# Kernel optimization log

Measured on AMD Instinct MI355X. Metric: run time of the kernel, lower is better.

Reference implementation:

```python
import jax, jax.numpy as jnp
import numpy as np

B, T, J, C = 32, 256, 21, 3
BT = B * T
N = BT * J

_TPL_SRC = np.array([0, 1, 2, 3, 4, 0, 5, 6, 7, 8, 0, 9, 10, 11, 12, 0, 13, 14, 15, 16, 0, 17, 18, 19, 20], np.int32)
_TPL_DST = np.array([1, 2, 3, 4, 0, 5, 6, 7, 8, 0, 9, 10, 11, 12, 0, 13, 14, 15, 16, 0, 17, 18, 19, 20, 0], np.int32)


def _build_edges():
    off = (np.arange(BT, dtype=np.int32) * J)[:, None]
    src = (_TPL_SRC[None, :] + off).ravel()
    dst = (_TPL_DST[None, :] + off).ravel()
    # PyG GATConv default add_self_loops=True (both layers see the same augmented set)
    loops = np.arange(N, dtype=np.int32)
    return np.concatenate([src, loops]), np.concatenate([dst, loops])


def setup_inputs() -> dict:
    key = jax.random.key(0)
    ks = jax.random.split(key, 8)
    src, dst = _build_edges()
    return {
        "keypoints": jax.random.normal(ks[0], (B, T, J, C), jnp.float32),
        "W1": jax.random.normal(ks[1], (3, 256), jnp.float32) * 0.3,
        "att1_src": jax.random.normal(ks[2], (4, 64), jnp.float32) * 0.1,
        "att1_dst": jax.random.normal(ks[3], (4, 64), jnp.float32) * 0.1,
        "b1": jnp.zeros((256,), jnp.float32),
        "W2": jax.random.normal(ks[4], (256, 128), jnp.float32) * 0.06,
        "att2_src": jax.random.normal(ks[5], (1, 128), jnp.float32) * 0.1,
        "att2_dst": jax.random.normal(ks[6], (1, 128), jnp.float32) * 0.1,
        "b2": jnp.zeros((128,), jnp.float32),
        "src": jnp.asarray(src),
        "dst": jnp.asarray(dst),
    }


def _gat_conv(x, src, dst, W, a_src, a_dst, b, heads, d_head):
    n = x.shape[0]
    h = (x @ W).reshape(n, heads, d_head)            # [N,H,D]
    e_s = jnp.einsum('nhd,hd->nh', h, a_src)          # [N,H]
    e_d = jnp.einsum('nhd,hd->nh', h, a_dst)
    e = jax.nn.leaky_relu(e_s[src] + e_d[dst], 0.2)   # [E,H]
    m = jax.ops.segment_max(e, dst, num_segments=n)
    ex = jnp.exp(e - m[dst])
    z = jax.ops.segment_sum(ex, dst, num_segments=n)
    alpha = ex / z[dst]                               # scatter-softmax over dst
    out = jax.ops.segment_sum(h[src] * alpha[:, :, None], dst, num_segments=n)
    return out.reshape(n, heads * d_head) + b


def reference(keypoints, W1, att1_src, att1_dst, b1, W2, att2_src, att2_dst, b2, src, dst):
    x = keypoints.reshape(N, C)
    x = jax.nn.relu(_gat_conv(x, src, dst, W1, att1_src, att1_dst, b1, 4, 64))
    x = jax.nn.relu(_gat_conv(x, src, dst, W2, att2_src, att2_dst, b2, 1, 128))
    x = x.reshape(BT, J, 128).mean(axis=1)            # pool joints
    return x.reshape(B, T, 128).mean(axis=1)          # pool time -> [B,128]
```

## Files before the change

kernel.cpp:

```cpp
#include <hip/hip_runtime.h>

#define NJ  21
#define X1S 264
#define H2S 132
#define XAS 40

typedef __attribute__((ext_vector_type(8))) short  bf16x8;
typedef __attribute__((ext_vector_type(4))) float  floatx4;

__device__ __forceinline__ float lrelu(float v){ return v > 0.f ? v : 0.2f*v; }
__device__ __forceinline__ unsigned short f2bf(float x){
  unsigned int u = __float_as_uint(x);
  return (unsigned short)((u + 0x7FFFu + ((u >> 16) & 1u)) >> 16);
}
__device__ __forceinline__ unsigned short f2bf_u(float x){
  return (unsigned short)((__float_as_uint(x) + 0x8000u) >> 16);
}

__global__ void prep(const float* __restrict__ W1, const float* __restrict__ a1s,
                     const float* __restrict__ a1d, const float* __restrict__ W2,
                     unsigned short* __restrict__ w2f, unsigned short* __restrict__ w1b,
                     float* __restrict__ ws1o, float* __restrict__ out){
  const int t = threadIdx.x, b = blockIdx.x;
  if (b < 32){
    int base = b*1024 + t*4;
    #pragma unroll
    for (int i = 0; i < 4; ++i){
      int idx = base + i;
      int j = idx & 7, lane = (idx >> 3) & 63, nt = (idx >> 9) & 7, kt = idx >> 12;
      int k = kt*32 + (lane >> 4)*8 + j;
      int n = nt*16 + (lane & 15);
      w2f[idx] = f2bf(W2[k*128 + n]);
    }
  } else if (b < 40){
    int base = (b - 32)*1024 + t*4;
    #pragma unroll
    for (int i = 0; i < 4; ++i){
      int idx = base + i;
      int j = idx & 7, lane = (idx >> 3) & 63, nt = idx >> 9;
      int k = (lane >> 4)*8 + j;
      int n = nt*16 + (lane & 15);
      float v = 0.f;
      if (k < 16){
        int h = k >> 2, c = k & 3;
        if (c < 3 && h == (n >> 6)) v = W1[c*256 + n];
      }
      w1b[idx] = f2bf(v);
    }
  } else {
    if (t < 24){
      int c = t % 3, h = (t/3) & 3, sd = t/12;
      const float* av = sd ? a1d : a1s;
      float s = 0.f;
      #pragma unroll
      for (int d = 0; d < 64; ++d) s += W1[c*256 + h*64 + d]*av[h*64 + d];
      ws1o[sd*12 + c*4 + h] = s;
    }
    for (int i = t; i < 4096; i += 256) out[i] = 0.f;
  }
}

__global__ __launch_bounds__(256, 5)
void gat_fused(const float* __restrict__ kp,  const float* __restrict__ b1v,
               const float* __restrict__ a2s, const float* __restrict__ a2d,
               const float* __restrict__ b2v, const unsigned short* __restrict__ w2f,
               const unsigned short* __restrict__ w1b, const float* __restrict__ ws1g,
               float* __restrict__ out)
{
  __shared__ float xsL[2][NJ][4];
  __shared__ unsigned short xagb[48*XAS] __attribute__((aligned(16)));
  __shared__ float a2sL[128], a2dL[128];
  __shared__ unsigned short x1bf[48*X1S] __attribute__((aligned(16)));
  float* h2f = (float*)x1bf;
  float* esL = (float*)xagb;
  float* edL = (float*)((char*)xagb + 176);
  float (*al2F)[NJ][8] = (float(*)[NJ][8])((char*)xagb + 352);

  const int t = threadIdx.x, blk = blockIdx.x;
  const int w = t >> 6, lane = t & 63, quad = lane >> 4, ln15 = lane & 15;
  const int h = t & 3;

  if (t < 126){ int fl = t >= 63; int r = t - 63*fl; xsL[fl][r/3][r%3] = kp[blk*126 + t]; }
  if (t < 128) a2sL[t] = a2s[t]; else a2dL[t-128] = a2d[t-128];
  __syncthreads();

  if (t < 168){
    int fn = t >> 2, fl = fn >= NJ, n = fn - fl*NJ;
    float wsr[3], wdr[3];
    #pragma unroll
    for (int c = 0; c < 3; ++c){ wsr[c] = ws1g[c*4 + h]; wdr[c] = ws1g[12 + c*4 + h]; }
    int p[6], np;
    if (n == 0){ p[0]=4;p[1]=8;p[2]=12;p[3]=16;p[4]=20;p[5]=0; np=6; }
    else       { p[0]=(n%4==1)?0:(n-1); p[1]=n; np=2; }
    float4 xself = *(const float4*)&xsL[fl][n][0];
    float ed = xself.x*wdr[0] + xself.y*wdr[1] + xself.z*wdr[2];
    float4 xp[6]; float e[6]; float m = -1e30f;
    for (int i = 0; i < np; ++i){
      xp[i] = *(const float4*)&xsL[fl][p[i]][0];
      float es = xp[i].x*wsr[0] + xp[i].y*wsr[1] + xp[i].z*wsr[2];
      e[i] = lrelu(es + ed); m = fmaxf(m, e[i]);
    }
    float z = 0.f;
    for (int i = 0; i < np; ++i){ e[i] = __expf(e[i]-m); z += e[i]; }
    float inv = 1.f/z;
    float a0 = 0.f, a1 = 0.f, a2v = 0.f;
    for (int i = 0; i < np; ++i){
      float al = e[i]*inv;
      a0 += al*xp[i].x; a1 += al*xp[i].y; a2v += al*xp[i].z;
    }
    uint2 pk;
    pk.x = (unsigned)f2bf(a0) | ((unsigned)f2bf(a1) << 16);
    pk.y = (unsigned)f2bf(a2v);
    *(uint2*)&xagb[fn*XAS + h*4] = pk;
    uint2 z2; z2.x = 0u; z2.y = 0u;
    *(uint2*)&xagb[fn*XAS + 16 + h*4] = z2;
  }
  __syncthreads();

  {
    bf16x8 A0 = *(bf16x8*)&xagb[(     ln15)*XAS + quad*8];
    bf16x8 A1 = *(bf16x8*)&xagb[(16 + ln15)*XAS + quad*8];
    bf16x8 A2 = *(bf16x8*)&xagb[(32 + ln15)*XAS + quad*8];
    bf16x8 Bv[4]; float bb[4];
    #pragma unroll
    for (int i = 0; i < 4; ++i){
      Bv[i] = *(const bf16x8*)(w1b + (unsigned)((w*4 + i)*64 + lane)*8);
      bb[i] = b1v[w*64 + i*16 + ln15];
    }
    #pragma unroll
    for (int i = 0; i < 4; ++i){
      const int cb = w*64 + i*16 + ln15;
      floatx4 c0 = {0.f,0.f,0.f,0.f}, c1 = c0, c2 = c0;
      c0 = __builtin_amdgcn_mfma_f32_16x16x32_bf16(A0, Bv[i], c0, 0,0,0);
      c1 = __builtin_amdgcn_mfma_f32_16x16x32_bf16(A1, Bv[i], c1, 0,0,0);
      c2 = __builtin_amdgcn_mfma_f32_16x16x32_bf16(A2, Bv[i], c2, 0,0,0);
      #pragma unroll
      for (int r = 0; r < 4; ++r){
        x1bf[(     quad*4 + r)*X1S + cb] = f2bf_u(fmaxf(c0[r] + bb[i], 0.f));
        x1bf[(16 + quad*4 + r)*X1S + cb] = f2bf_u(fmaxf(c1[r] + bb[i], 0.f));
        x1bf[(32 + quad*4 + r)*X1S + cb] = f2bf_u(fmaxf(c2[r] + bb[i], 0.f));
      }
    }
  }
  __syncthreads();

  floatx4 acc[3][2];
  #pragma unroll
  for (int mt = 0; mt < 3; ++mt){ acc[mt][0] = (floatx4){0.f,0.f,0.f,0.f}; acc[mt][1] = acc[mt][0]; }
  {
    #define LDA(row0, kt) (*(bf16x8*)&x1bf[((row0) + ln15)*X1S + (kt)*32 + quad*8])
    #define LDB(kt, half) (*(const bf16x8*)(w2f + (unsigned)(((kt)*8 + 2*w + (half))*64 + lane)*8))
    bf16x8 A0c = LDA(0,0), A1c = LDA(16,0), A2c = LDA(32,0);
    bf16x8 B0s[3], B1s[3];
    #pragma unroll
    for (int i = 0; i < 3; ++i){ B0s[i] = LDB(i,0); B1s[i] = LDB(i,1); }
    #pragma unroll
    for (int kt = 0; kt < 8; ++kt){
      bf16x8 b0c = B0s[kt%3], b1c = B1s[kt%3];
      bf16x8 A0n, A1n, A2n;
      if (kt < 7){ A0n = LDA(0,kt+1); A1n = LDA(16,kt+1); A2n = LDA(32,kt+1); }
      if (kt < 5){ B0s[kt%3] = LDB(kt+3,0); B1s[kt%3] = LDB(kt+3,1); }
      acc[0][0] = __builtin_amdgcn_mfma_f32_16x16x32_bf16(A0c, b0c, acc[0][0], 0,0,0);
      acc[0][1] = __builtin_amdgcn_mfma_f32_16x16x32_bf16(A0c, b1c, acc[0][1], 0,0,0);
      acc[1][0] = __builtin_amdgcn_mfma_f32_16x16x32_bf16(A1c, b0c, acc[1][0], 0,0,0);
      acc[1][1] = __builtin_amdgcn_mfma_f32_16x16x32_bf16(A1c, b1c, acc[1][1], 0,0,0);
      acc[2][0] = __builtin_amdgcn_mfma_f32_16x16x32_bf16(A2c, b0c, acc[2][0], 0,0,0);
      acc[2][1] = __builtin_amdgcn_mfma_f32_16x16x32_bf16(A2c, b1c, acc[2][1], 0,0,0);
      if (kt < 7){ A0c = A0n; A1c = A1n; A2c = A2n; }
    }
    #undef LDA
    #undef LDB
  }
  __syncthreads();
  {
    const int c0 = 32*w + ln15, c1 = c0 + 16;
    #pragma unroll
    for (int mt = 0; mt < 3; ++mt){
      #pragma unroll
      for (int r = 0; r < 4; ++r){
        int row = mt*16 + quad*4 + r;
        if (row < 42){
          h2f[row*H2S + c0] = acc[mt][0][r];
          h2f[row*H2S + c1] = acc[mt][1][r];
        }
      }
    }
  }
  __syncthreads();

  if (w < 2){
    const int fl = w;
    float s = 0.f, d = 0.f;
    if (lane < 42){
      int n = lane >> 1, cb2 = (lane & 1)*64;
      const float* hp  = h2f + (fl*NJ + n)*H2S + cb2;
      const float* asp = a2sL + cb2;
      const float* adp = a2dL + cb2;
      #pragma unroll
      for (int c = 0; c < 64; c += 4){
        float4 hv = *(const float4*)(hp + c);
        float4 av = *(const float4*)(asp + c);
        float4 dv = *(const float4*)(adp + c);
        s += hv.x*av.x + hv.y*av.y + hv.z*av.z + hv.w*av.w;
        d += hv.x*dv.x + hv.y*dv.y + hv.z*dv.z + hv.w*dv.w;
      }
    }
    s += __shfl_xor(s, 1); d += __shfl_xor(d, 1);
    if (lane < 42 && (lane & 1) == 0){ esL[fl*NJ + (lane>>1)] = s; edL[fl*NJ + (lane>>1)] = d; }
    __threadfence_block();
    if (lane < NJ){
      int n = lane;
      int p[6], np;
      if (n == 0){ p[0]=4;p[1]=8;p[2]=12;p[3]=16;p[4]=20;p[5]=0; np=6; }
      else       { p[0]=(n%4==1)?0:(n-1); p[1]=n; np=2; }
      float ed = edL[fl*NJ + n];
      float e[6], m = -1e30f;
      for (int i = 0; i < np; ++i){ e[i] = lrelu(esL[fl*NJ + p[i]] + ed); m = fmaxf(m, e[i]); }
      float z = 0.f;
      for (int i = 0; i < np; ++i){ e[i] = __expf(e[i]-m); z += e[i]; }
      float inv = 1.f/z;
      for (int i = 0; i < np; ++i) al2F[fl][n][i] = e[i]*inv;
    }
    __threadfence_block();
    #pragma unroll
    for (int jj = 0; jj < 2; ++jj){
      int j = lane + jj*64;
      float bj = b2v[j];
      float h0 = h2f[(fl*NJ)*H2S + j];
      float v0 = al2F[fl][0][5]*h0;
      float sum = 0.f, hprev = h0;
      #pragma unroll
      for (int n = 1; n < NJ; ++n){
        float hn = h2f[(fl*NJ + n)*H2S + j];
        float pv = ((n & 3) == 1) ? h0 : hprev;
        float2 al = *(const float2*)&al2F[fl][n][0];
        sum += fmaxf(bj + al.x*pv + al.y*hn, 0.f);
        if ((n & 3) == 0) v0 += al2F[fl][0][(n >> 2) - 1]*hn;
        hprev = hn;
      }
      sum += fmaxf(bj + v0, 0.f);
      atomicAdd(&out[(blk >> 7)*128 + j], sum*(1.f/5376.f));
    }
  }
}

extern "C" void kernel_launch(void* const* d_in, const int* in_sizes, int n_in,
                              void* d_out, int out_size, void* d_ws, size_t ws_size,
                              hipStream_t stream){
  const float* kp  = (const float*)d_in[0];
  const float* W1  = (const float*)d_in[1];
  const float* a1s = (const float*)d_in[2];
  const float* a1d = (const float*)d_in[3];
  const float* b1  = (const float*)d_in[4];
  const float* W2  = (const float*)d_in[5];
  const float* a2s = (const float*)d_in[6];
  const float* a2d = (const float*)d_in[7];
  const float* b2  = (const float*)d_in[8];
  float* out = (float*)d_out;

  unsigned short* w2f = (unsigned short*)d_ws;
  unsigned short* w1b = (unsigned short*)((char*)d_ws + 65536);
  float* ws1 = (float*)((char*)d_ws + 65536 + 16384);

  prep<<<41, 256, 0, stream>>>(W1, a1s, a1d, W2, w2f, w1b, ws1, out);
  gat_fused<<<4096, 256, 0, stream>>>(kp, b1, a2s, a2d, b2, w2f, w1b, ws1, out);
}
```

Baseline: 139.9 us.

## Restructure GAT kernel to one wave per frame with barrier-free execution

Each block is now a single 64-thread wave that processes one frame of 21 joints, where before it was four waves handling two frames. All __syncthreads become __threadfence_block, and the wave computes the full 256-wide layer-1 output and all 128 layer-2 columns with 16 accumulators. The aim is to remove block-level barriers and pad waste (48 rows down to 32), and to raise the number of independent blocks. In exchange, each wave reloads all of W2 from global or L2 with no split across waves, and register pressure rises. Atomic contention on the output also doubles.

New measurement: 185.6 us. 32.7% more time.

```diff
diff --git a/kernel.cpp b/kernel.cpp
--- a/kernel.cpp
+++ b/kernel.cpp
@@ -60,142 +60,117 @@
   }
 }
 
-__global__ __launch_bounds__(256, 5)
+__global__ __launch_bounds__(64, 3)
 void gat_fused(const float* __restrict__ kp,  const float* __restrict__ b1v,
                const float* __restrict__ a2s, const float* __restrict__ a2d,
                const float* __restrict__ b2v, const unsigned short* __restrict__ w2f,
                const unsigned short* __restrict__ w1b, const float* __restrict__ ws1g,
                float* __restrict__ out)
 {
-  __shared__ float xsL[2][NJ][4];
-  __shared__ unsigned short xagb[48*XAS] __attribute__((aligned(16)));
-  __shared__ float a2sL[128], a2dL[128];
-  __shared__ unsigned short x1bf[48*X1S] __attribute__((aligned(16)));
+  __shared__ unsigned short x1bf[NJ*X1S] __attribute__((aligned(16)));
+  __shared__ float xs[NJ][4];
+  __shared__ unsigned short xagb[32*XAS] __attribute__((aligned(16)));
+  __shared__ float esL[NJ], edL[NJ];
+  __shared__ float al2[NJ][6];
   float* h2f = (float*)x1bf;
-  float* esL = (float*)xagb;
-  float* edL = (float*)((char*)xagb + 176);
-  float (*al2F)[NJ][8] = (float(*)[NJ][8])((char*)xagb + 352);
-
-  const int t = threadIdx.x, blk = blockIdx.x;
-  const int w = t >> 6, lane = t & 63, quad = lane >> 4, ln15 = lane & 15;
-  const int h = t & 3;
-
-  if (t < 126){ int fl = t >= 63; int r = t - 63*fl; xsL[fl][r/3][r%3] = kp[blk*126 + t]; }
-  if (t < 128) a2sL[t] = a2s[t]; else a2dL[t-128] = a2d[t-128];
-  __syncthreads();
-
-  if (t < 168){
-    int fn = t >> 2, fl = fn >= NJ, n = fn - fl*NJ;
-    float wsr[3], wdr[3];
-    #pragma unroll
-    for (int c = 0; c < 3; ++c){ wsr[c] = ws1g[c*4 + h]; wdr[c] = ws1g[12 + c*4 + h]; }
+
+  const int lane = threadIdx.x, blk = blockIdx.x;
+  const int quad = lane >> 4, ln15 = lane & 15;
+
+  if (lane < 63) xs[lane/3][lane%3] = kp[blk*63 + lane];
+  __threadfence_block();
+
+  if (lane < NJ){
+    const int n = lane;
     int p[6], np;
     if (n == 0){ p[0]=4;p[1]=8;p[2]=12;p[3]=16;p[4]=20;p[5]=0; np=6; }
     else       { p[0]=(n%4==1)?0:(n-1); p[1]=n; np=2; }
-    float4 xself = *(const float4*)&xsL[fl][n][0];
-    float ed = xself.x*wdr[0] + xself.y*wdr[1] + xself.z*wdr[2];
-    float4 xp[6]; float e[6]; float m = -1e30f;
-    for (int i = 0; i < np; ++i){
-      xp[i] = *(const float4*)&xsL[fl][p[i]][0];
-      float es = xp[i].x*wsr[0] + xp[i].y*wsr[1] + xp[i].z*wsr[2];
-      e[i] = lrelu(es + ed); m = fmaxf(m, e[i]);
-    }
-    float z = 0.f;
-    for (int i = 0; i < np; ++i){ e[i] = __expf(e[i]-m); z += e[i]; }
-    float inv = 1.f/z;
-    float a0 = 0.f, a1 = 0.f, a2v = 0.f;
-    for (int i = 0; i < np; ++i){
-      float al = e[i]*inv;
-      a0 += al*xp[i].x; a1 += al*xp[i].y; a2v += al*xp[i].z;
-    }
-    uint2 pk;
-    pk.x = (unsigned)f2bf(a0) | ((unsigned)f2bf(a1) << 16);
-    pk.y = (unsigned)f2bf(a2v);
-    *(uint2*)&xagb[fn*XAS + h*4] = pk;
-    uint2 z2; z2.x = 0u; z2.y = 0u;
-    *(uint2*)&xagb[fn*XAS + 16 + h*4] = z2;
-  }
-  __syncthreads();
+    float4 xself = *(const float4*)&xs[n][0];
+    float4 xp[6];
+    for (int i = 0; i < np; ++i) xp[i] = *(const float4*)&xs[p[i]][0];
+    #pragma unroll
+    for (int h = 0; h < 4; ++h){
+      float wsr0 = ws1g[h],    wsr1 = ws1g[4+h],  wsr2 = ws1g[8+h];
+      float wdr0 = ws1g[12+h], wdr1 = ws1g[16+h], wdr2 = ws1g[20+h];
+      float ed = xself.x*wdr0 + xself.y*wdr1 + xself.z*wdr2;
+      float e[6], m = -1e30f;
+      for (int i = 0; i < np; ++i){
+        e[i] = lrelu(xp[i].x*wsr0 + xp[i].y*wsr1 + xp[i].z*wsr2 + ed);
+        m = fmaxf(m, e[i]);
+      }
+      float z = 0.f;
+      for (int i = 0; i < np; ++i){ e[i] = __expf(e[i]-m); z += e[i]; }
+      float inv = 1.f/z;
+      float a0 = 0.f, a1 = 0.f, a2v = 0.f;
+      for (int i = 0; i < np; ++i){
+        float al = e[i]*inv;
+        a0 += al*xp[i].x; a1 += al*xp[i].y; a2v += al*xp[i].z;
+      }
+      uint2 pk;
+      pk.x = (unsigned)f2bf(a0) | ((unsigned)f2bf(a1) << 16);
+      pk.y = (unsigned)f2bf(a2v);
+      *(uint2*)&xagb[n*XAS + h*4] = pk;
+      uint2 zz; zz.x = 0u; zz.y = 0u;
+      *(uint2*)&xagb[n*XAS + 16 + h*4] = zz;
+    }
+  }
+  __threadfence_block();
 
   {
     bf16x8 A0 = *(bf16x8*)&xagb[(     ln15)*XAS + quad*8];
     bf16x8 A1 = *(bf16x8*)&xagb[(16 + ln15)*XAS + quad*8];
-    bf16x8 A2 = *(bf16x8*)&xagb[(32 + ln15)*XAS + quad*8];
-    bf16x8 Bv[4]; float bb[4];
-    #pragma unroll
-    for (int i = 0; i < 4; ++i){
-      Bv[i] = *(const bf16x8*)(w1b + (unsigned)((w*4 + i)*64 + lane)*8);
-      bb[i] = b1v[w*64 + i*16 + ln15];
-    }
-    #pragma unroll
-    for (int i = 0; i < 4; ++i){
-      const int cb = w*64 + i*16 + ln15;
-      floatx4 c0 = {0.f,0.f,0.f,0.f}, c1 = c0, c2 = c0;
-      c0 = __builtin_amdgcn_mfma_f32_16x16x32_bf16(A0, Bv[i], c0, 0,0,0);
-      c1 = __builtin_amdgcn_mfma_f32_16x16x32_bf16(A1, Bv[i], c1, 0,0,0);
-      c2 = __builtin_amdgcn_mfma_f32_16x16x32_bf16(A2, Bv[i], c2, 0,0,0);
+    #pragma unroll
+    for (int nt = 0; nt < 16; ++nt){
+      bf16x8 Bv = *(const bf16x8*)(w1b + (unsigned)((nt*64 + lane)*8));
+      floatx4 c0 = {0.f,0.f,0.f,0.f}, c1 = c0;
+      c0 = __builtin_amdgcn_mfma_f32_16x16x32_bf16(A0, Bv, c0, 0,0,0);
+      c1 = __builtin_amdgcn_mfma_f32_16x16x32_bf16(A1, Bv, c1, 0,0,0);
+      const int cb = nt*16 + ln15;
+      float bb = b1v[cb];
       #pragma unroll
       for (int r = 0; r < 4; ++r){
-        x1bf[(     quad*4 + r)*X1S + cb] = f2bf_u(fmaxf(c0[r] + bb[i], 0.f));
-        x1bf[(16 + quad*4 + r)*X1S + cb] = f2bf_u(fmaxf(c1[r] + bb[i], 0.f));
-        x1bf[(32 + quad*4 + r)*X1S + cb] = f2bf_u(fmaxf(c2[r] + bb[i], 0.f));
-      }
-    }
-  }
-  __syncthreads();
-
-  floatx4 acc[3][2];
-  #pragma unroll
-  for (int mt = 0; mt < 3; ++mt){ acc[mt][0] = (floatx4){0.f,0.f,0.f,0.f}; acc[mt][1] = acc[mt][0]; }
+        x1bf[(quad*4 + r)*X1S + cb] = f2bf_u(fmaxf(c0[r] + bb, 0.f));
+        int r1 = 16 + quad*4 + r;
+        if (r1 < NJ) x1bf[r1*X1S + cb] = f2bf_u(fmaxf(c1[r] + bb, 0.f));
+      }
+    }
+  }
+  __threadfence_block();
+
+  const int row1 = (ln15 < 5) ? (16 + ln15) : ln15;
+  floatx4 acc0[8], acc1[8];
+  #pragma unroll
+  for (int nt = 0; nt < 8; ++nt){ acc0[nt] = (floatx4){0.f,0.f,0.f,0.f}; acc1[nt] = acc0[nt]; }
+  #pragma unroll
+  for (int kt = 0; kt < 8; ++kt){
+    bf16x8 a0 = *(bf16x8*)&x1bf[ln15*X1S + kt*32 + quad*8];
+    bf16x8 a1 = *(bf16x8*)&x1bf[row1*X1S + kt*32 + quad*8];
+    #pragma unroll
+    for (int nt = 0; nt < 8; ++nt){
+      bf16x8 b = *(const bf16x8*)(w2f + (unsigned)(((kt*8 + nt)*64 + lane)*8));
+      acc0[nt] = __builtin_amdgcn_mfma_f32_16x16x32_bf16(a0, b, acc0[nt], 0,0,0);
+      acc1[nt] = __builtin_amdgcn_mfma_f32_16x16x32_bf16(a1, b, acc1[nt], 0,0,0);
+    }
+  }
+  #pragma unroll
+  for (int nt = 0; nt < 8; ++nt){
+    const int c = nt*16 + ln15;
+    #pragma unroll
+    for (int r = 0; r < 4; ++r){
+      h2f[(quad*4 + r)*H2S + c] = acc0[nt][r];
+      int r1s = 16 + quad*4 + r;
+      if (r1s < NJ) h2f[r1s*H2S + c] = acc1[nt][r];
+    }
+  }
+  __threadfence_block();
+
   {
-    #define LDA(row0, kt) (*(bf16x8*)&x1bf[((row0) + ln15)*X1S + (kt)*32 + quad*8])
-    #define LDB(kt, half) (*(const bf16x8*)(w2f + (unsigned)(((kt)*8 + 2*w + (half))*64 + lane)*8))
-    bf16x8 A0c = LDA(0,0), A1c = LDA(16,0), A2c = LDA(32,0);
-    bf16x8 B0s[3], B1s[3];
-    #pragma unroll
-    for (int i = 0; i < 3; ++i){ B0s[i] = LDB(i,0); B1s[i] = LDB(i,1); }
-    #pragma unroll
-    for (int kt = 0; kt < 8; ++kt){
-      bf16x8 b0c = B0s[kt%3], b1c = B1s[kt%3];
-      bf16x8 A0n, A1n, A2n;
-      if (kt < 7){ A0n = LDA(0,kt+1); A1n = LDA(16,kt+1); A2n = LDA(32,kt+1); }
-      if (kt < 5){ B0s[kt%3] = LDB(kt+3,0); B1s[kt%3] = LDB(kt+3,1); }
-      acc[0][0] = __builtin_amdgcn_mfma_f32_16x16x32_bf16(A0c, b0c, acc[0][0], 0,0,0);
-      acc[0][1] = __builtin_amdgcn_mfma_f32_16x16x32_bf16(A0c, b1c, acc[0][1], 0,0,0);
-      acc[1][0] = __builtin_amdgcn_mfma_f32_16x16x32_bf16(A1c, b0c, acc[1][0], 0,0,0);
-      acc[1][1] = __builtin_amdgcn_mfma_f32_16x16x32_bf16(A1c, b1c, acc[1][1], 0,0,0);
-      acc[2][0] = __builtin_amdgcn_mfma_f32_16x16x32_bf16(A2c, b0c, acc[2][0], 0,0,0);
-      acc[2][1] = __builtin_amdgcn_mfma_f32_16x16x32_bf16(A2c, b1c, acc[2][1], 0,0,0);
-      if (kt < 7){ A0c = A0n; A1c = A1n; A2c = A2n; }
-    }
-    #undef LDA
-    #undef LDB
-  }
-  __syncthreads();
-  {
-    const int c0 = 32*w + ln15, c1 = c0 + 16;
-    #pragma unroll
-    for (int mt = 0; mt < 3; ++mt){
-      #pragma unroll
-      for (int r = 0; r < 4; ++r){
-        int row = mt*16 + quad*4 + r;
-        if (row < 42){
-          h2f[row*H2S + c0] = acc[mt][0][r];
-          h2f[row*H2S + c1] = acc[mt][1][r];
-        }
-      }
-    }
-  }
-  __syncthreads();
-
-  if (w < 2){
-    const int fl = w;
     float s = 0.f, d = 0.f;
     if (lane < 42){
       int n = lane >> 1, cb2 = (lane & 1)*64;
-      const float* hp  = h2f + (fl*NJ + n)*H2S + cb2;
-      const float* asp = a2sL + cb2;
-      const float* adp = a2dL + cb2;
+      const float* hp  = h2f + n*H2S + cb2;
+      const float* asp = a2s + cb2;
+      const float* adp = a2d + cb2;
       #pragma unroll
       for (int c = 0; c < 64; c += 4){
         float4 hv = *(const float4*)(hp + c);
@@ -206,41 +181,43 @@
       }
     }
     s += __shfl_xor(s, 1); d += __shfl_xor(d, 1);
-    if (lane < 42 && (lane & 1) == 0){ esL[fl*NJ + (lane>>1)] = s; edL[fl*NJ + (lane>>1)] = d; }
-    __threadfence_block();
-    if (lane < NJ){
-      int n = lane;
-      int p[6], np;
-      if (n == 0){ p[0]=4;p[1]=8;p[2]=12;p[3]=16;p[4]=20;p[5]=0; np=6; }
-      else       { p[0]=(n%4==1)?0:(n-1); p[1]=n; np=2; }
-      float ed = edL[fl*NJ + n];
-      float e[6], m = -1e30f;
-      for (int i = 0; i < np; ++i){ e[i] = lrelu(esL[fl*NJ + p[i]] + ed); m = fmaxf(m, e[i]); }
-      float z = 0.f;
-      for (int i = 0; i < np; ++i){ e[i] = __expf(e[i]-m); z += e[i]; }
-      float inv = 1.f/z;
-      for (int i = 0; i < np; ++i) al2F[fl][n][i] = e[i]*inv;
-    }
-    __threadfence_block();
-    #pragma unroll
-    for (int jj = 0; jj < 2; ++jj){
-      int j = lane + jj*64;
-      float bj = b2v[j];
-      float h0 = h2f[(fl*NJ)*H2S + j];
-      float v0 = al2F[fl][0][5]*h0;
-      float sum = 0.f, hprev = h0;
-      #pragma unroll
-      for (int n = 1; n < NJ; ++n){
-        float hn = h2f[(fl*NJ + n)*H2S + j];
-        float pv = ((n & 3) == 1) ? h0 : hprev;
-        float2 al = *(const float2*)&al2F[fl][n][0];
-        sum += fmaxf(bj + al.x*pv + al.y*hn, 0.f);
-        if ((n & 3) == 0) v0 += al2F[fl][0][(n >> 2) - 1]*hn;
-        hprev = hn;
-      }
-      sum += fmaxf(bj + v0, 0.f);
-      atomicAdd(&out[(blk >> 7)*128 + j], sum*(1.f/5376.f));
-    }
+    if (lane < 42 && (lane & 1) == 0){ esL[lane>>1] = s; edL[lane>>1] = d; }
+  }
+  __threadfence_block();
+
+  if (lane < NJ){
+    const int n = lane;
+    int p[6], np;
+    if (n == 0){ p[0]=4;p[1]=8;p[2]=12;p[3]=16;p[4]=20;p[5]=0; np=6; }
+    else       { p[0]=(n%4==1)?0:(n-1); p[1]=n; np=2; }
+    float ed = edL[n];
+    float e[6], m = -1e30f;
+    for (int i = 0; i < np; ++i){ e[i] = lrelu(esL[p[i]] + ed); m = fmaxf(m, e[i]); }
+    float z = 0.f;
+    for (int i = 0; i < np; ++i){ e[i] = __expf(e[i]-m); z += e[i]; }
+    float inv = 1.f/z;
+    for (int i = 0; i < np; ++i) al2[n][i] = e[i]*inv;
+  }
+  __threadfence_block();
+
+  #pragma unroll
+  for (int jj = 0; jj < 2; ++jj){
+    const int j = lane + jj*64;
+    float bj = b2v[j];
+    float h0 = h2f[j];
+    float v0 = al2[0][5]*h0;
+    float s = 0.f, hprev = h0;
+    #pragma unroll
+    for (int n = 1; n < NJ; ++n){
+      float hn = h2f[n*H2S + j];
+      float pv = ((n & 3) == 1) ? h0 : hprev;
+      float2 al = *(const float2*)&al2[n][0];
+      s += fmaxf(bj + al.x*pv + al.y*hn, 0.f);
+      if ((n & 3) == 0) v0 += al2[0][(n >> 2) - 1]*hn;
+      hprev = hn;
+    }
+    s += fmaxf(bj + v0, 0.f);
+    atomicAdd(&out[(blk >> 8)*128 + j], s*(1.f/5376.f));
   }
 }
 
@@ -263,5 +240,5 @@
   float* ws1 = (float*)((char*)d_ws + 65536 + 16384);
 
   prep<<<41, 256, 0, stream>>>(W1, a1s, a1d, W2, w2f, w1b, ws1, out);
-  gat_fused<<<4096, 256, 0, stream>>>(kp, b1, a2s, a2d, b2, w2f, w1b, ws1, out);
-}
+  gat_fused<<<8192, 64, 0, stream>>>(kp, b1, a2s, a2d, b2, w2f, w1b, ws1, out);
+}
```
